# Kernel optimization log

Measured on AMD Instinct MI355X. Metric: run time of the kernel, lower is better.

## Reference

```python
import jax, jax.numpy as jnp
import numpy as np
import math
from jax import lax

B, HS, WS, C, T, TD, HH, TOPM = 8, 64, 64, 512, 77, 512, 8, 3
DH = C // HH
CONF_TH = 0.35


def _layernorm(x, w, b, eps=1e-5):
    mu = x.mean(-1, keepdims=True)
    var = ((x - mu) ** 2).mean(-1, keepdims=True)
    return (x - mu) * lax.rsqrt(var + eps) * w + b


def _l2norm(x, eps=1e-6):
    n = jnp.sqrt((x * x).sum(-1, keepdims=True))
    return x / jnp.maximum(n, eps)


def _forward(visual_features, text_features, geo_mask,
             ln1_w, ln1_b, wq, bq, wk, bk, wv, bv, wo, bo,
             gate_w, gate_b, logit_scale, alpha,
             ln2_w, ln2_b, ffn_w1, ffn_b1, ffn_w2, ffn_b2):
    Bb, Hs, Ws, Cv = visual_features.shape
    N = Hs * Ws
    # Pre-LN + flatten spatial
    x = _layernorm(visual_features, ln1_w, ln1_b).reshape(Bb, N, Cv)
    q_full = x @ wq + bq                                  # [B,N,C]
    pad_mask = jnp.abs(text_features).sum(-1) <= 1e-6     # [B,T]
    k_full = text_features @ wk + bk                      # [B,T,C]
    v_full = text_features @ wv + bv
    # per-token L2 normalize over full channel dim, then split heads
    q = _l2norm(q_full).reshape(Bb, N, HH, DH)
    k = _l2norm(k_full).reshape(Bb, T, HH, DH)
    v = v_full.reshape(Bb, T, HH, DH)
    scale = jnp.exp(jnp.clip(logit_scale, -2.0, 2.0)) / jnp.sqrt(jnp.float32(DH))
    sim = jnp.einsum('bnhd,bthd->bnht', q, k) * scale     # [B,N,H,T]
    # geo gate (4D tensor branch): log-bias on logits + multiplicative channel gate later
    gate_map = jnp.clip(geo_mask, 0.3, 1.0)               # [B,1,Hs,Ws]
    geo_gate_flat = gate_map.reshape(Bb, N, 1)            # [B,N,1]
    sim = sim + jnp.log(jnp.maximum(gate_map.reshape(Bb, N), 1e-6))[:, :, None, None]
    sim = jnp.where(pad_mask[:, None, None, :], -jnp.inf, sim)
    # Top-K sparsification before softmax (threshold at the K-th value)
    topv = lax.top_k(sim, TOPM)[0]                        # [B,N,H,K]
    sim = jnp.where(sim >= topv[..., -1:], sim, -jnp.inf)
    attn = jax.nn.softmax(sim, axis=-1)
    attn = attn / jnp.maximum(attn.sum(-1, keepdims=True), 1e-6)
    # fully-padded rows -> zero
    all_pad = pad_mask.all(axis=1)
    attn = jnp.where(all_pad[:, None, None, None], 0.0, attn)
    # confidence bypass: conf = max_prob * (1 - normalized entropy), mean over heads
    a_hn = attn.transpose(0, 2, 1, 3)                     # [B,H,N,T]
    maxp = a_hn.max(-1, keepdims=True)
    t_eff = jnp.maximum((a_hn > 0).astype(a_hn.dtype).sum(-1, keepdims=True), 2.0)
    p = jnp.maximum(a_hn, 1e-8)
    ent = jnp.maximum(-(p * jnp.log(p)).sum(-1, keepdims=True) / jnp.log(t_eff), 0.0)
    conf = jnp.clip(maxp * (1.0 - ent), 0.0, 1.0).mean(axis=1)   # [B,N,1]
    conf_scale = CONF_TH + (1.0 - CONF_TH) * jnp.clip(conf, 0.0, 1.0)
    aligned = jnp.einsum('bnht,bthd->bnhd', attn, v).reshape(Bb, N, HH * DH)
    aligned = (aligned @ wo + bo) * conf_scale
    gate = jax.nn.sigmoid(x @ gate_w + gate_b) * geo_gate_flat
    y = x + alpha * gate * aligned
    h = _layernorm(y, ln2_w, ln2_b)
    y = y + (jax.nn.gelu(h @ ffn_w1 + ffn_b1, approximate=False) @ ffn_w2 + ffn_b2)
    return y.reshape(Bb, Hs, Ws, Cv)


def setup_inputs() -> dict:
    key = jax.random.key(0)
    ks = jax.random.split(key, 16)
    def w(k, shp, fan_in):
        return (jax.random.normal(k, shp, jnp.float32) * (1.0 / math.sqrt(fan_in))).astype(jnp.float32)
    return {
        'visual_features': jax.random.normal(ks[0], (B, HS, WS, C), jnp.float32),
        'text_features':   jax.random.normal(ks[1], (B, T, TD), jnp.float32),
        'geo_mask':        jax.random.uniform(ks[2], (B, 1, HS, WS), jnp.float32),
        'ln1_w': jnp.ones((C,), jnp.float32), 'ln1_b': jnp.zeros((C,), jnp.float32),
        'wq': w(ks[3], (C, C), C),   'bq': jnp.zeros((C,), jnp.float32),
        'wk': w(ks[4], (TD, C), TD), 'bk': jnp.zeros((C,), jnp.float32),
        'wv': w(ks[5], (TD, C), TD), 'bv': jnp.zeros((C,), jnp.float32),
        'wo': w(ks[6], (C, C), C),   'bo': jnp.zeros((C,), jnp.float32),
        'gate_w': w(ks[7], (C, C), C), 'gate_b': jnp.zeros((C,), jnp.float32),
        'logit_scale': jnp.float32(math.log(1.0 / 0.07)),
        'alpha': jnp.float32(0.1),
        'ln2_w': jnp.ones((C,), jnp.float32), 'ln2_b': jnp.zeros((C,), jnp.float32),
        'ffn_w1': w(ks[8], (C, 4 * C), C),    'ffn_b1': jnp.zeros((4 * C,), jnp.float32),
        'ffn_w2': w(ks[9], (4 * C, C), 4 * C), 'ffn_b2': jnp.zeros((C,), jnp.float32),
    }


def reference(visual_features, text_features, geo_mask,
              ln1_w, ln1_b, wq, bq, wk, bk, wv, bv, wo, bo,
              gate_w, gate_b, logit_scale, alpha,
              ln2_w, ln2_b, ffn_w1, ffn_b1, ffn_w2, ffn_b2):
    return _forward(visual_features, text_features, geo_mask,
                    ln1_w, ln1_b, wq, bq, wk, bk, wv, bv, wo, bo,
                    gate_w, gate_b, logit_scale, alpha,
                    ln2_w, ln2_b, ffn_w1, ffn_b1, ffn_w2, ffn_b2)
```

## Files before the change

### kernel.cpp

```cpp
#include <hip/hip_runtime.h>
#include <hip/hip_bf16.h>
#include <math.h>

#define TT 77
#define MTOT 32768

typedef __attribute__((ext_vector_type(8))) short bf16x8;
typedef __attribute__((ext_vector_type(4))) float floatx4;

#define GPTR(p) ((const __attribute__((address_space(1))) void*)(p))
#define LPTR(p) ((__attribute__((address_space(3))) void*)(p))

__device__ __forceinline__ float wred_sum(float v) {
#pragma unroll
  for (int o = 32; o >= 1; o >>= 1) v += __shfl_xor(v, o, 64);
  return v;
}

__device__ __forceinline__ unsigned short f2bf(float f) {
  unsigned int u = __float_as_uint(f);
  unsigned int r = (u + 0x7fffu + ((u >> 16) & 1u)) >> 16;
  return (unsigned short)r;
}
__device__ __forceinline__ float bf2f(unsigned short h) {
  return __uint_as_float(((unsigned int)h) << 16);
}
__device__ __forceinline__ unsigned int cvt2bf(float a, float b) {
  unsigned int r;
  asm("v_cvt_pk_bf16_f32 %0, %1, %2" : "=v"(r) : "v"(a), "v"(b));
  return r;
}

__device__ __forceinline__ float fast_gelu(float o) {
  const float z = fabsf(o) * 0.70710678118654752f;
  const float t = __builtin_amdgcn_rcpf(fmaf(0.3275911f, z, 1.0f));
  float p = fmaf(1.061405429f, t, -1.453152027f);
  p = fmaf(p, t, 1.421413741f);
  p = fmaf(p, t, -0.284496736f);
  p = fmaf(p, t, 0.254829592f);
  p = p * t;
  const float erfz = fmaf(-p, __expf(-z * z), 1.0f);
  const float s = __builtin_copysignf(erfz, o);
  return 0.5f * o * (1.0f + s);
}

__device__ __forceinline__ float fast_sigmoid(float o) {
  return __builtin_amdgcn_rcpf(1.0f + __expf(-o));
}

__global__ __launch_bounds__(256)
void ln_bf16_kernel(const float* __restrict__ in, const float* __restrict__ gw,
                    const float* __restrict__ gb, unsigned short* __restrict__ out) {
  const int wv = threadIdx.x >> 6, lane = threadIdx.x & 63;
  const size_t row = (size_t)blockIdx.x * 4 + wv;
  const float* p = in + row * 512 + lane * 8;
  float4 a = *(const float4*)p;
  float4 b = *(const float4*)(p + 4);
  float s = a.x + a.y + a.z + a.w + b.x + b.y + b.z + b.w;
  float mu = wred_sum(s) * (1.0f / 512.0f);
  float d[8] = {a.x - mu, a.y - mu, a.z - mu, a.w - mu,
                b.x - mu, b.y - mu, b.z - mu, b.w - mu};
  float ss = 0.f;
#pragma unroll
  for (int i = 0; i < 8; ++i) ss = fmaf(d[i], d[i], ss);
  float var = wred_sum(ss) * (1.0f / 512.0f);
  float rstd = rsqrtf(var + 1e-5f);
  float4 w0 = *(const float4*)(gw + lane * 8);
  float4 w1 = *(const float4*)(gw + lane * 8 + 4);
  float4 c0 = *(const float4*)(gb + lane * 8);
  float4 c1 = *(const float4*)(gb + lane * 8 + 4);
  float o[8];
  o[0] = d[0] * rstd * w0.x + c0.x;  o[1] = d[1] * rstd * w0.y + c0.y;
  o[2] = d[2] * rstd * w0.z + c0.z;  o[3] = d[3] * rstd * w0.w + c0.w;
  o[4] = d[4] * rstd * w1.x + c1.x;  o[5] = d[5] * rstd * w1.y + c1.y;
  o[6] = d[6] * rstd * w1.z + c1.z;  o[7] = d[7] * rstd * w1.w + c1.w;
  __align__(16) unsigned short ob[8];
#pragma unroll
  for (int i = 0; i < 8; ++i) ob[i] = f2bf(o[i]);
  *(uint4*)(out + row * 512 + lane * 8) = *(const uint4*)ob;
}

__global__ __launch_bounds__(256)
void zero_ss_kernel(float* __restrict__ ssq) {
  ssq[blockIdx.x * 256 + threadIdx.x] = 0.0f;
}

__global__ __launch_bounds__(256)
void transpose_bf16_kernel(const float* __restrict__ W, unsigned short* __restrict__ WTb,
                           int K, int N) {
  __shared__ float s[32][33];
  const int tx = threadIdx.x & 31, ty = threadIdx.x >> 5;
  const int n0 = blockIdx.x * 32, k0 = blockIdx.y * 32;
#pragma unroll
  for (int j = 0; j < 4; ++j)
    s[ty + 8 * j][tx] = W[(size_t)(k0 + ty + 8 * j) * N + n0 + tx];
  __syncthreads();
#pragma unroll
  for (int j = 0; j < 4; ++j)
    WTb[(size_t)(n0 + ty + 8 * j) * K + k0 + tx] = f2bf(s[tx][ty + 8 * j]);
}

__global__ __launch_bounds__(256)
void transpose_pair_kernel(const float* __restrict__ W,
                           unsigned short* __restrict__ WTh,
                           unsigned short* __restrict__ WTl, int K, int N) {
  __shared__ float s[32][33];
  const int tx = threadIdx.x & 31, ty = threadIdx.x >> 5;
  const int n0 = blockIdx.x * 32, k0 = blockIdx.y * 32;
#pragma unroll
  for (int j = 0; j < 4; ++j)
    s[ty + 8 * j][tx] = W[(size_t)(k0 + ty + 8 * j) * N + n0 + tx];
  __syncthreads();
#pragma unroll
  for (int j = 0; j < 4; ++j) {
    const float a = s[tx][ty + 8 * j];
    const unsigned short hi = f2bf(a);
    WTh[(size_t)(n0 + ty + 8 * j) * K + k0 + tx] = hi;
    WTl[(size_t)(n0 + ty + 8 * j) * K + k0 + tx] = f2bf(a - bf2f(hi));
  }
}

__global__ __launch_bounds__(256)
void text_cvt_kernel(const float* __restrict__ text,
                     unsigned short* __restrict__ thi,
                     unsigned short* __restrict__ tlo,
                     float* __restrict__ negm) {
  const int wv = threadIdx.x >> 6, lane = threadIdx.x & 63;
  const int row = blockIdx.x * 4 + wv;
  if (row >= 616) {
    const uint4 z = {0u, 0u, 0u, 0u};
    *(uint4*)(thi + (size_t)row * 512 + lane * 8) = z;
    *(uint4*)(tlo + (size_t)row * 512 + lane * 8) = z;
    return;
  }
  const float* p = text + (size_t)row * 512 + lane * 8;
  float4 a = *(const float4*)p;
  float4 b = *(const float4*)(p + 4);
  float v[8] = {a.x, a.y, a.z, a.w, b.x, b.y, b.z, b.w};
  float ab = 0.f;
#pragma unroll
  for (int i = 0; i < 8; ++i) ab += fabsf(v[i]);
  ab = wred_sum(ab);
  __align__(16) unsigned short hb[8];
  __align__(16) unsigned short lb[8];
#pragma unroll
  for (int i = 0; i < 8; ++i) {
    hb[i] = f2bf(v[i]);
    lb[i] = f2bf(v[i] - bf2f(hb[i]));
  }
  *(uint4*)(thi + (size_t)row * 512 + lane * 8) = *(const uint4*)hb;
  *(uint4*)(tlo + (size_t)row * 512 + lane * 8) = *(const uint4*)lb;
  if (lane == 0) {
    const int bb = row / 77, t = row - bb * 77;
    negm[bb * 80 + t] = (ab <= 1e-6f) ? -INFINITY : 0.0f;
  }
}

__global__ __launch_bounds__(256)
void kv_gemm(const unsigned short* __restrict__ AH,
             const unsigned short* __restrict__ AL,
             const unsigned short* __restrict__ BH,
             const unsigned short* __restrict__ BL,
             const float* __restrict__ bk, const float* __restrict__ bv,
             float* __restrict__ outp) {
  const int K = 512;
  __shared__ __align__(16) unsigned short AsH[128 * 32];
  __shared__ __align__(16) unsigned short AsL[128 * 32];
  __shared__ __align__(16) unsigned short BsH[128 * 32];
  __shared__ __align__(16) unsigned short BsL[128 * 32];
  const int tid = threadIdx.x;
  const int wid = tid >> 6, lane = tid & 63;
  const int wr = wid >> 1, wc = wid & 1;
  const int m16 = lane & 15, quad = lane >> 4;
  const int row0 = blockIdx.y * 128, col0 = blockIdx.x * 128;

  const floatx4 zero4 = {0.f, 0.f, 0.f, 0.f};
  floatx4 acc[4][4];
#pragma unroll
  for (int i = 0; i < 4; ++i)
#pragma unroll
    for (int j = 0; j < 4; ++j) acc[i][j] = zero4;

  const int srow = tid >> 2;
  const int schunk = (tid & 3) ^ (srow & 3);
  const unsigned short* AgH = AH + (size_t)(row0 + srow) * K + schunk * 8;
  const unsigned short* AgL = AL + (size_t)(row0 + srow) * K + schunk * 8;
  const unsigned short* BgH = BH + (size_t)(col0 + srow) * K + schunk * 8;
  const unsigned short* BgL = BL + (size_t)(col0 + srow) * K + schunk * 8;
  char* AsHB = (char*)AsH + tid * 16;
  char* AsLB = (char*)AsL + tid * 16;
  char* BsHB = (char*)BsH + tid * 16;
  char* BsLB = (char*)BsL + tid * 16;
  const int rq = quad ^ (m16 & 3);
  const int aOfs = (wr * 64 + m16) * 32 + rq * 8;
  const int bOfs = (wc * 64 + m16) * 32 + rq * 8;

  for (int k0 = 0; k0 < K; k0 += 32) {
    __syncthreads();
    __builtin_amdgcn_global_load_lds(GPTR(AgH + k0), LPTR(AsHB), 16, 0, 0);
    __builtin_amdgcn_global_load_lds(GPTR(AgH + (size_t)64 * K + k0), LPTR(AsHB + 4096), 16, 0, 0);
    __builtin_amdgcn_global_load_lds(GPTR(AgL + k0), LPTR(AsLB), 16, 0, 0);
    __builtin_amdgcn_global_load_lds(GPTR(AgL + (size_t)64 * K + k0), LPTR(AsLB + 4096), 16, 0, 0);
    __builtin_amdgcn_global_load_lds(GPTR(BgH + k0), LPTR(BsHB), 16, 0, 0);
    __builtin_amdgcn_global_load_lds(GPTR(BgH + (size_t)64 * K + k0), LPTR(BsHB + 4096), 16, 0, 0);
    __builtin_amdgcn_global_load_lds(GPTR(BgL + k0), LPTR(BsLB), 16, 0, 0);
    __builtin_amdgcn_global_load_lds(GPTR(BgL + (size_t)64 * K + k0), LPTR(BsLB + 4096), 16, 0, 0);
    __syncthreads();
    bf16x8 afH[4], afL[4], bfH[4], bfL[4];
#pragma unroll
    for (int i = 0; i < 4; ++i) {
      afH[i] = *(const bf16x8*)(AsH + aOfs + i * 16 * 32);
      afL[i] = *(const bf16x8*)(AsL + aOfs + i * 16 * 32);
      bfH[i] = *(const bf16x8*)(BsH + bOfs + i * 16 * 32);
      bfL[i] = *(const bf16x8*)(BsL + bOfs + i * 16 * 32);
    }
#pragma unroll
    for (int mi = 0; mi < 4; ++mi)
#pragma unroll
      for (int ni = 0; ni < 4; ++ni) {
        acc[mi][ni] = __builtin_amdgcn_mfma_f32_16x16x32_bf16(afH[mi], bfH[ni], acc[mi][ni], 0, 0, 0);
        acc[mi][ni] = __builtin_amdgcn_mfma_f32_16x16x32_bf16(afH[mi], bfL[ni], acc[mi][ni], 0, 0, 0);
        acc[mi][ni] = __builtin_amdgcn_mfma_f32_16x16x32_bf16(afL[mi], bfH[ni], acc[mi][ni], 0, 0, 0);
      }
  }

  const float* bp = (col0 < 512) ? bk : bv;
  const int cbase = (col0 < 512) ? col0 : col0 - 512;
  float bb[4];
#pragma unroll
  for (int ni = 0; ni < 4; ++ni) bb[ni] = bp[cbase + wc * 64 + ni * 16 + m16];
#pragma unroll
  for (int mi = 0; mi < 4; ++mi)
#pragma unroll
    for (int r = 0; r < 4; ++r) {
      const int row = row0 + wr * 64 + mi * 16 + quad * 4 + r;
#pragma unroll
      for (int ni = 0; ni < 4; ++ni) {
        const int col = col0 + wc * 64 + ni * 16 + m16;
        outp[(size_t)row * 1024 + col] = acc[mi][ni][r] + bb[ni];
      }
    }
}

__global__ __launch_bounds__(256)
void knorm_kernel(const float* __restrict__ KV,
                  unsigned short* __restrict__ khb) {
  const int wv = threadIdx.x >> 6, lane = threadIdx.x & 63;
  const int row = blockIdx.x * 4 + wv;
  const float* p = KV + (size_t)row * 1024 + lane * 8;
  float4 a = *(const float4*)p;
  float4 b = *(const float4*)(p + 4);
  float v[8] = {a.x, a.y, a.z, a.w, b.x, b.y, b.z, b.w};
  float ss = 0.f;
#pragma unroll
  for (int i = 0; i < 8; ++i) ss = fmaf(v[i], v[i], ss);
  ss = wred_sum(ss);
  const float sc = 1.0f / fmaxf(sqrtf(ss), 1e-6f);
  const int bb = row / 77, t = row - bb * 77;
  const int c = lane * 8, h = c >> 6, d = c & 63;
  __align__(16) unsigned short ob[8];
#pragma unroll
  for (int i = 0; i < 8; ++i) ob[i] = f2bf(v[i] * sc);
  *(uint4*)(khb + (((size_t)bb * 8 + h) * 80 + t) * 64 + d) = *(const uint4*)ob;
}

__global__ __launch_bounds__(256)
void kpad_zero_kernel(unsigned short* __restrict__ khb, float* __restrict__ negm) {
  const int i = blockIdx.x * 256 + threadIdx.x;
  const int bh = i / 192, rem = i - bh * 192;
  const int t = 77 + rem / 64, d = rem & 63;
  khb[(((size_t)bh) * 80 + t) * 64 + d] = 0;
  if (i < 24) negm[(i / 3) * 80 + 77 + (i % 3)] = -INFINITY;
}

__global__ __launch_bounds__(256)
void sim_kernel(const unsigned short* __restrict__ qnb,
                const unsigned short* __restrict__ khb,
                const float* __restrict__ negm,
                const float* __restrict__ ssq,
                const float* __restrict__ logit_scale,
                float* __restrict__ SIM) {
  __shared__ __align__(16) unsigned short As[128 * 72];
  __shared__ __align__(16) unsigned short Bs[80 * 72];
  const int bh = blockIdx.y;
  const int b = bh >> 3, h = bh & 7;
  const int row0 = blockIdx.x * 128;
  const int tid = threadIdx.x;
  {
    const int r = tid >> 1, half = tid & 1;
    const unsigned short* src = qnb + ((size_t)b * 4096 + row0 + r) * 512 + h * 64 + half * 32;
    unsigned short* dst = As + r * 72 + half * 32;
    *(uint4*)dst = *(const uint4*)src;
    *(uint4*)(dst + 8) = *(const uint4*)(src + 8);
    *(uint4*)(dst + 16) = *(const uint4*)(src + 16);
    *(uint4*)(dst + 24) = *(const uint4*)(src + 24);
  }
  if (tid < 160) {
    const int r = tid >> 1, half = tid & 1;
    const unsigned short* src = khb + ((size_t)bh * 80 + r) * 64 + half * 32;
    unsigned short* dst = Bs + r * 72 + half * 32;
    *(uint4*)dst = *(const uint4*)src;
    *(uint4*)(dst + 8) = *(const uint4*)(src + 8);
    *(uint4*)(dst + 16) = *(const uint4*)(src + 16);
    *(uint4*)(dst + 24) = *(const uint4*)(src + 24);
  }
  __syncthreads();
  const int w = tid >> 6, lane = tid & 63;
  const int m16 = lane & 15, quad = lane >> 4;
  const unsigned short* aBase = As + (w * 32 + m16) * 72 + quad * 8;
  const unsigned short* bBase = Bs + m16 * 72 + quad * 8;
  bf16x8 af[2][2], bf[5][2];
#pragma unroll
  for (int mi = 0; mi < 2; ++mi)
#pragma unroll
    for (int kk = 0; kk < 2; ++kk)
      af[mi][kk] = *(const bf16x8*)(aBase + mi * 16 * 72 + kk * 32);
#pragma unroll
  for (int ni = 0; ni < 5; ++ni)
#pragma unroll
    for (int kk = 0; kk < 2; ++kk)
      bf[ni][kk] = *(const bf16x8*)(bBase + ni * 16 * 72 + kk * 32);
  const floatx4 zero4 = {0.f, 0.f, 0.f, 0.f};
  floatx4 acc[2][5];
#pragma unroll
  for (int mi = 0; mi < 2; ++mi)
#pragma unroll
    for (int ni = 0; ni < 5; ++ni) acc[mi][ni] = zero4;
#pragma unroll
  for (int kk = 0; kk < 2; ++kk)
#pragma unroll
    for (int mi = 0; mi < 2; ++mi)
#pragma unroll
      for (int ni = 0; ni < 5; ++ni)
        acc[mi][ni] = __builtin_amdgcn_mfma_f32_16x16x32_bf16(af[mi][kk], bf[ni][kk], acc[mi][ni], 0, 0, 0);
  const float ls = fminf(fmaxf(logit_scale[0], -2.0f), 2.0f);
  const float scale = expf(ls) * 0.125f;
  float nm[5];
#pragma unroll
  for (int ni = 0; ni < 5; ++ni) nm[ni] = negm[b * 80 + ni * 16 + m16];
  float* obase = SIM + ((size_t)bh * 4096 + row0 + w * 32 + quad * 4) * 80 + m16;
#pragma unroll
  for (int mi = 0; mi < 2; ++mi)
#pragma unroll
    for (int r = 0; r < 4; ++r) {
      const int rl = row0 + w * 32 + quad * 4 + mi * 16 + r;
      const float ssv = ssq[(size_t)b * 4096 + rl];
      const float nsc = scale / fmaxf(sqrtf(ssv), 1e-6f);
#pragma unroll
      for (int ni = 0; ni < 5; ++ni)
        obase[(size_t)(mi * 16 + r) * 80 + ni * 16] = acc[mi][ni][r] * nsc + nm[ni];
    }
}

__global__ __launch_bounds__(256)
void attn_topk_pv_kernel(const float* __restrict__ SIM,
                         const float* __restrict__ vf,
                         unsigned short* __restrict__ alignedb,
                         float* __restrict__ conf_out) {
  const int g = blockIdx.x * 256 + threadIdx.x;
  const int b = g >> 15;
  const int local = g & 32767;
  const int n = local >> 3, h = local & 7;
  const float* sp = SIM + ((size_t)(b * 8 + h) * 4096 + n) * 80;

  float m1 = -INFINITY, m2 = -INFINITY, m3 = -INFINITY, m4 = -INFINITY;
  int a1 = 0, a2 = 0, a3 = 0;
#pragma unroll
  for (int i = 0; i < 20; ++i) {
    const float4 q = ((const float4*)sp)[i];
#pragma unroll
    for (int j = 0; j < 4; ++j) {
      const float v = (j == 0) ? q.x : (j == 1) ? q.y : (j == 2) ? q.z : q.w;
      const int t = i * 4 + j;
      const bool c1 = v > m1, c2 = v > m2, c3 = v > m3, c4 = v > m4;
      m4 = c4 ? (c3 ? m3 : v) : m4;
      m3 = c3 ? (c2 ? m2 : v) : m3;
      a3 = c3 ? (c2 ? a2 : t) : a3;
      m2 = c2 ? (c1 ? m1 : v) : m2;
      a2 = c2 ? (c1 ? a1 : t) : a2;
      m1 = c1 ? v : m1;
      a1 = c1 ? t : a1;
    }
  }

  const bool dead = (m1 == -INFINITY);
  if (dead) m1 = 0.0f;
  const bool tie = (!dead) && ((m1 == m2) || (m2 == m3) || (m3 == m4));

  const float d2 = m2 - m1, d3 = m3 - m1;
  const float e2 = __expf(d2), e3 = __expf(d3);
  float s0 = 1.0f + e2 + e3;
  float s1 = ((e2 > 0.f) ? e2 * d2 : 0.f) + ((e3 > 0.f) ? e3 * d3 : 0.f);
  float cntf = 1.0f + ((e2 > 0.f) ? 1.f : 0.f) + ((e3 > 0.f) ? 1.f : 0.f);

  const float w1 = dead ? 0.f : 1.f;
  const float* v1p = vf + (size_t)(b * 77 + a1) * 1024 + h * 64;
  const float* v2p = vf + (size_t)(b * 77 + a2) * 1024 + h * 64;
  const float* v3p = vf + (size_t)(b * 77 + a3) * 1024 + h * 64;
  float4 acc[16];
#pragma unroll
  for (int i = 0; i < 16; ++i) {
    const float4 x1 = ((const float4*)v1p)[i];
    const float4 x2 = ((const float4*)v2p)[i];
    const float4 x3 = ((const float4*)v3p)[i];
    float4 r;
    r.x = fmaf(e3, x3.x, fmaf(e2, x2.x, w1 * x1.x));
    r.y = fmaf(e3, x3.y, fmaf(e2, x2.y, w1 * x1.y));
    r.z = fmaf(e3, x3.z, fmaf(e2, x2.z, w1 * x1.z));
    r.w = fmaf(e3, x3.w, fmaf(e2, x2.w, w1 * x1.w));
    acc[i] = r;
  }

  if (__any(tie)) {
    if (tie) {
      s0 = 0.f; s1 = 0.f; cntf = 0.f;
#pragma unroll
      for (int i = 0; i < 16; ++i) acc[i] = (float4){0.f, 0.f, 0.f, 0.f};
      for (int t = 0; t < 80; ++t) {
        const float v = sp[t];
        if (v >= m3) {
          const float e = expf(v - m1);
          if (e > 0.f) {
            s0 += e; s1 = fmaf(e, v - m1, s1); cntf += 1.f;
            const float4* vp = (const float4*)(vf + (size_t)(b * 77 + t) * 1024 + h * 64);
#pragma unroll
            for (int i = 0; i < 16; ++i) {
              const float4 x = vp[i];
              acc[i].x = fmaf(e, x.x, acc[i].x);
              acc[i].y = fmaf(e, x.y, acc[i].y);
              acc[i].z = fmaf(e, x.z, acc[i].z);
              acc[i].w = fmaf(e, x.w, acc[i].w);
            }
          }
        }
      }
    }
  }

  const float inv = 1.0f / s0;
  const float entn = (__logf(s0) - s1 * inv) + (77.0f - cntf) * 1.8420681e-7f;
  const float ent = fmaxf(entn / __logf(fmaxf(cntf, 2.0f)), 0.0f);
  float conf_h = fminf(fmaxf(inv * (1.0f - ent), 0.0f), 1.0f);
  if (dead) conf_h = 0.f;
  float cs = conf_h;
  cs += __shfl_xor(cs, 1, 64);
  cs += __shfl_xor(cs, 2, 64);
  cs += __shfl_xor(cs, 4, 64);
  if (h == 0) {
    const float cm = fminf(fmaxf(cs * 0.125f, 0.0f), 1.0f);
    conf_out[(size_t)b * 4096 + n] = 0.35f + 0.65f * cm;
  }

  unsigned short* op = alignedb + ((size_t)b * 4096 + n) * 512 + h * 64;
#pragma unroll
  for (int i = 0; i < 8; ++i) {
    const float4 lo = acc[2 * i], hi = acc[2 * i + 1];
    uint4 pk;
    pk.x = cvt2bf(lo.x * inv, lo.y * inv);
    pk.y = cvt2bf(lo.z * inv, lo.w * inv);
    pk.z = cvt2bf(hi.x * inv, hi.y * inv);
    pk.w = cvt2bf(hi.z * inv, hi.w * inv);
    *(uint4*)(op + i * 8) = pk;
  }
}

template <int EPI, int KC>
__global__ __launch_bounds__(256)
void mfma_gemm(const unsigned short* __restrict__ A,
               const unsigned short* __restrict__ WT,
               const float* __restrict__ bias,
               void* __restrict__ outv, int M, int N,
               const unsigned short* __restrict__ e0b,
               const float* __restrict__ e1f,
               const float* __restrict__ e2f,
               const float* __restrict__ scf) {
  __shared__ __align__(16) unsigned short As[128 * 32];
  __shared__ __align__(16) unsigned short Bs[128 * 32];
  const int tid = threadIdx.x;
  const int wid = tid >> 6, lane = tid & 63;
  const int wr = wid >> 1, wc = wid & 1;
  const int m16 = lane & 15, quad = lane >> 4;

  const int nwg = gridDim.x * gridDim.y;
  const int orig = blockIdx.y * gridDim.x + blockIdx.x;
  const int qq = nwg >> 3, rr = nwg & 7;
  const int xcd = orig & 7, base = orig >> 3;
  const int logical = (xcd < rr ? xcd * (qq + 1) : rr * (qq + 1) + (xcd - rr) * qq) + base;
  const int bx = logical % gridDim.x, by = logical / gridDim.x;
  const int row0 = by * 128, col0 = bx * 128;

  const floatx4 zero4 = {0.f, 0.f, 0.f, 0.f};
  floatx4 acc[4][4];
#pragma unroll
  for (int i = 0; i < 4; ++i)
#pragma unroll
    for (int j = 0; j < 4; ++j) acc[i][j] = zero4;

  const int srow = tid >> 2;
  const int schunk = (tid & 3) ^ (srow & 3);
  const unsigned short* Ag = A + (size_t)(row0 + srow) * KC + schunk * 8;
  const unsigned short* Bg = WT + (size_t)(col0 + srow) * KC + schunk * 8;
  char* AsB = (char*)As + tid * 16;
  char* BsB = (char*)Bs + tid * 16;
  const int rq = quad ^ (m16 & 3);
  const unsigned short* aP = As + (wr * 64 + m16) * 32 + rq * 8;
  const unsigned short* bP = Bs + (wc * 64 + m16) * 32 + rq * 8;

  for (int k0 = 0; k0 < KC; k0 += 32) {
    __syncthreads();
    __builtin_amdgcn_global_load_lds(GPTR(Ag + k0), LPTR(AsB), 16, 0, 0);
    __builtin_amdgcn_global_load_lds(GPTR(Ag + (size_t)64 * KC + k0), LPTR(AsB + 4096), 16, 0, 0);
    __builtin_amdgcn_global_load_lds(GPTR(Bg + k0), LPTR(BsB), 16, 0, 0);
    __builtin_amdgcn_global_load_lds(GPTR(Bg + (size_t)64 * KC + k0), LPTR(BsB + 4096), 16, 0, 0);
    __syncthreads();
    bf16x8 af[4], bfr[4];
#pragma unroll
    for (int i = 0; i < 4; ++i) {
      af[i] = *(const bf16x8*)(aP + i * 16 * 32);
      bfr[i] = *(const bf16x8*)(bP + i * 16 * 32);
    }
#pragma unroll
    for (int mi = 0; mi < 4; ++mi)
#pragma unroll
      for (int ni = 0; ni < 4; ++ni)
        acc[mi][ni] = __builtin_amdgcn_mfma_f32_16x16x32_bf16(af[mi], bfr[ni], acc[mi][ni], 0, 0, 0);
  }

  float* outf = (float*)outv;
  unsigned short* outb = (unsigned short*)outv;
  const unsigned short* albf = (const unsigned short*)e1f;
  float bb[4];
#pragma unroll
  for (int ni = 0; ni < 4; ++ni) bb[ni] = bias[col0 + wc * 64 + ni * 16 + m16];
  const float alphav = (EPI == 2) ? scf[0] : 0.f;

#pragma unroll
  for (int mi = 0; mi < 4; ++mi) {
#pragma unroll
    for (int r = 0; r < 4; ++r) {
      const int row = row0 + wr * 64 + mi * 16 + quad * 4 + r;
      float o[4];
#pragma unroll
      for (int ni = 0; ni < 4; ++ni) o[ni] = acc[mi][ni][r] + bb[ni];
      const size_t basei = (size_t)row * N + col0 + wc * 64 + m16;

      if (EPI == 5) {
        const unsigned int p01 = cvt2bf(o[0], o[1]);
        const unsigned int p23 = cvt2bf(o[2], o[3]);
        outb[basei] = (unsigned short)p01;
        outb[basei + 16] = (unsigned short)(p01 >> 16);
        outb[basei + 32] = (unsigned short)p23;
        outb[basei + 48] = (unsigned short)(p23 >> 16);
        float p = fmaf(o[0], o[0], fmaf(o[1], o[1], fmaf(o[2], o[2], o[3] * o[3])));
        p += __shfl_xor(p, 1, 64);
        p += __shfl_xor(p, 2, 64);
        p += __shfl_xor(p, 4, 64);
        p += __shfl_xor(p, 8, 64);
        if (m16 == 0) atomicAdd(const_cast<float*>(e1f) + row, p);
      } else if (EPI == 3) {
        const unsigned int p01 = cvt2bf(fast_gelu(o[0]), fast_gelu(o[1]));
        const unsigned int p23 = cvt2bf(fast_gelu(o[2]), fast_gelu(o[3]));
        outb[basei] = (unsigned short)p01;
        outb[basei + 16] = (unsigned short)(p01 >> 16);
        outb[basei + 32] = (unsigned short)p23;
        outb[basei + 48] = (unsigned short)(p23 >> 16);
      } else if (EPI == 1) {
        const float rowscale = e1f[row];
        const unsigned int p01 = cvt2bf(o[0] * rowscale, o[1] * rowscale);
        const unsigned int p23 = cvt2bf(o[2] * rowscale, o[3] * rowscale);
        outb[basei] = (unsigned short)p01;
        outb[basei + 16] = (unsigned short)(p01 >> 16);
        outb[basei + 32] = (unsigned short)p23;
        outb[basei + 48] = (unsigned short)(p23 >> 16);
      } else if (EPI == 2) {
        const float geo = fminf(fmaxf(e2f[row], 0.3f), 1.0f);
#pragma unroll
        for (int ni = 0; ni < 4; ++ni) {
          const size_t idx = basei + ni * 16;
          const float x = bf2f(e0b[idx]);
          const float al = bf2f(albf[idx]);
          const float sg = fast_sigmoid(o[ni]);
          outf[idx] = x + alphav * sg * geo * al;
        }
      } else {
#pragma unroll
        for (int ni = 0; ni < 4; ++ni) {
          const size_t idx = basei + ni * 16;
          outf[idx] = o[ni] + e1f[idx];
        }
      }
    }
  }
}

extern "C" void kernel_launch(void* const* d_in, const int* in_sizes, int n_in,
                              void* d_out, int out_size, void* d_ws, size_t ws_size,
                              hipStream_t stream) {
  const float* visual = (const float*)d_in[0];
  const float* text   = (const float*)d_in[1];
  const float* geo    = (const float*)d_in[2];
  const float* ln1_w  = (const float*)d_in[3];
  const float* ln1_b  = (const float*)d_in[4];
  const float* wq     = (const float*)d_in[5];
  const float* bq     = (const float*)d_in[6];
  const float* wk     = (const float*)d_in[7];
  const float* bk     = (const float*)d_in[8];
  const float* wvw    = (const float*)d_in[9];
  const float* bv     = (const float*)d_in[10];
  const float* wo     = (const float*)d_in[11];
  const float* bo     = (const float*)d_in[12];
  const float* gate_w = (const float*)d_in[13];
  const float* gate_b = (const float*)d_in[14];
  const float* logit_scale = (const float*)d_in[15];
  const float* alpha  = (const float*)d_in[16];
  const float* ln2_w  = (const float*)d_in[17];
  const float* ln2_b  = (const float*)d_in[18];
  const float* ffn_w1 = (const float*)d_in[19];
  const float* ffn_b1 = (const float*)d_in[20];
  const float* ffn_w2 = (const float*)d_in[21];
  const float* ffn_b2 = (const float*)d_in[22];
  float* out = (float*)d_out;

  char* ws = (char*)d_ws;
  float* R0            = (float*)ws;
  float* BUF2          = (float*)(ws + 88080384);
  unsigned short* Xb   = (unsigned short*)(ws + 155189248);
  unsigned short* QNb  = (unsigned short*)(ws + 188743680);
  unsigned short* wqT  = (unsigned short*)(ws + 222298112);
  unsigned short* woT  = wqT + 262144;
  unsigned short* gateT = woT + 262144;
  unsigned short* w1T  = gateT + 262144;
  unsigned short* w2T  = w1T + 1048576;
  unsigned short* KHb  = w2T + 1048576;
  float* NEGM = (float*)(ws + 230146048);
  float* CONF = (float*)(ws + 230148608);
  float* SSQ  = (float*)(ws + 230279680);

  float* KV            = (float*)(ws + 88080384);
  unsigned short* THi  = (unsigned short*)(ws + 88080384 + 2621440);
  unsigned short* TLo  = THi + 640 * 512;
  unsigned short* WKVh = TLo + 640 * 512;
  unsigned short* WKVl = WKVh + 1024 * 512;

  float* SIM = R0;
  unsigned short* ALb = QNb;

  transpose_bf16_kernel<<<dim3(16, 16), 256, 0, stream>>>(wq, wqT, 512, 512);
  transpose_bf16_kernel<<<dim3(16, 16), 256, 0, stream>>>(wo, woT, 512, 512);
  transpose_bf16_kernel<<<dim3(16, 16), 256, 0, stream>>>(gate_w, gateT, 512, 512);
  transpose_bf16_kernel<<<dim3(64, 16), 256, 0, stream>>>(ffn_w1, w1T, 512, 2048);
  transpose_bf16_kernel<<<dim3(16, 64), 256, 0, stream>>>(ffn_w2, w2T, 2048, 512);
  transpose_pair_kernel<<<dim3(16, 16), 256, 0, stream>>>(wk, WKVh, WKVl, 512, 512);
  transpose_pair_kernel<<<dim3(16, 16), 256, 0, stream>>>(wvw, WKVh + 512 * 512, WKVl + 512 * 512, 512, 512);

  ln_bf16_kernel<<<MTOT / 4, 256, 0, stream>>>(visual, ln1_w, ln1_b, Xb);
  zero_ss_kernel<<<128, 256, 0, stream>>>(SSQ);
  text_cvt_kernel<<<160, 256, 0, stream>>>(text, THi, TLo, NEGM);
  kv_gemm<<<dim3(8, 5), 256, 0, stream>>>(THi, TLo, WKVh, WKVl, bk, bv, KV);
  knorm_kernel<<<154, 256, 0, stream>>>(KV, KHb);
  kpad_zero_kernel<<<48, 256, 0, stream>>>(KHb, NEGM);
  mfma_gemm<5, 512><<<dim3(4, 256), 256, 0, stream>>>(Xb, wqT, bq, QNb, MTOT, 512,
                                                      nullptr, SSQ, nullptr, nullptr);
  sim_kernel<<<dim3(32, 64), 256, 0, stream>>>(QNb, KHb, NEGM, SSQ, logit_scale, SIM);
  attn_topk_pv_kernel<<<1024, 256, 0, stream>>>(SIM, KV + 512, ALb, CONF);
  unsigned short* AOb = (unsigned short*)R0;
  mfma_gemm<1, 512><<<dim3(4, 256), 256, 0, stream>>>(ALb, woT, bo, AOb, MTOT, 512,
                                                      nullptr, CONF, nullptr, nullptr);
  mfma_gemm<2, 512><<<dim3(4, 256), 256, 0, stream>>>(Xb, gateT, gate_b, BUF2, MTOT, 512,
                                                      Xb, (const float*)AOb, geo, alpha);
  ln_bf16_kernel<<<MTOT / 4, 256, 0, stream>>>(BUF2, ln2_w, ln2_b, Xb);
  unsigned short* GCH = (unsigned short*)R0;
  for (int ch = 0; ch < 2; ++ch) {
    const size_t off = (size_t)ch * 16384;
    mfma_gemm<3, 512><<<dim3(16, 128), 256, 0, stream>>>(Xb + off * 512, w1T, ffn_b1, GCH,
                                                         16384, 2048,
                                                         nullptr, nullptr, nullptr, nullptr);
    mfma_gemm<4, 2048><<<dim3(4, 128), 256, 0, stream>>>(GCH, w2T, ffn_b2, out + off * 512,
                                                         16384, 512,
                                                         nullptr, BUF2 + off * 512, nullptr, nullptr);
  }
}
```

Measured before the change: 606.2 us.

## Interleave SIM layout across heads and stream top-3 value gather

```diff
diff --git a/kernel.cpp b/kernel.cpp
--- a/kernel.cpp
+++ b/kernel.cpp
@@ -338,7 +338,8 @@
   float nm[5];
 #pragma unroll
   for (int ni = 0; ni < 5; ++ni) nm[ni] = negm[b * 80 + ni * 16 + m16];
-  float* obase = SIM + ((size_t)bh * 4096 + row0 + w * 32 + quad * 4) * 80 + m16;
+  float* obase = SIM + ((size_t)b * 4096 + row0 + w * 32 + quad * 4) * 640 + h * 4 + (m16 & 3);
+  const int jb = m16 >> 2;
 #pragma unroll
   for (int mi = 0; mi < 2; ++mi)
 #pragma unroll
@@ -348,7 +349,7 @@
       const float nsc = scale / fmaxf(sqrtf(ssv), 1e-6f);
 #pragma unroll
       for (int ni = 0; ni < 5; ++ni)
-        obase[(size_t)(mi * 16 + r) * 80 + ni * 16] = acc[mi][ni][r] * nsc + nm[ni];
+        obase[(size_t)(mi * 16 + r) * 640 + (ni * 4 + jb) * 32] = acc[mi][ni][r] * nsc + nm[ni];
     }
 }
 
@@ -361,13 +362,13 @@
   const int b = g >> 15;
   const int local = g & 32767;
   const int n = local >> 3, h = local & 7;
-  const float* sp = SIM + ((size_t)(b * 8 + h) * 4096 + n) * 80;
+  const float* sp = SIM + ((size_t)b * 4096 + n) * 640 + h * 4;
 
   float m1 = -INFINITY, m2 = -INFINITY, m3 = -INFINITY, m4 = -INFINITY;
   int a1 = 0, a2 = 0, a3 = 0;
 #pragma unroll
   for (int i = 0; i < 20; ++i) {
-    const float4 q = ((const float4*)sp)[i];
+    const float4 q = *(const float4*)(sp + i * 32);
 #pragma unroll
     for (int j = 0; j < 4; ++j) {
       const float v = (j == 0) ? q.x : (j == 1) ? q.y : (j == 2) ? q.z : q.w;
@@ -393,31 +394,16 @@
   float s1 = ((e2 > 0.f) ? e2 * d2 : 0.f) + ((e3 > 0.f) ? e3 * d3 : 0.f);
   float cntf = 1.0f + ((e2 > 0.f) ? 1.f : 0.f) + ((e3 > 0.f) ? 1.f : 0.f);
 
-  const float w1 = dead ? 0.f : 1.f;
-  const float* v1p = vf + (size_t)(b * 77 + a1) * 1024 + h * 64;
-  const float* v2p = vf + (size_t)(b * 77 + a2) * 1024 + h * 64;
-  const float* v3p = vf + (size_t)(b * 77 + a3) * 1024 + h * 64;
-  float4 acc[16];
-#pragma unroll
-  for (int i = 0; i < 16; ++i) {
-    const float4 x1 = ((const float4*)v1p)[i];
-    const float4 x2 = ((const float4*)v2p)[i];
-    const float4 x3 = ((const float4*)v3p)[i];
-    float4 r;
-    r.x = fmaf(e3, x3.x, fmaf(e2, x2.x, w1 * x1.x));
-    r.y = fmaf(e3, x3.y, fmaf(e2, x2.y, w1 * x1.y));
-    r.z = fmaf(e3, x3.z, fmaf(e2, x2.z, w1 * x1.z));
-    r.w = fmaf(e3, x3.w, fmaf(e2, x2.w, w1 * x1.w));
-    acc[i] = r;
-  }
+  unsigned short* op = alignedb + ((size_t)b * 4096 + n) * 512 + h * 64;
 
   if (__any(tie)) {
     if (tie) {
       s0 = 0.f; s1 = 0.f; cntf = 0.f;
+      float4 acc[16];
 #pragma unroll
       for (int i = 0; i < 16; ++i) acc[i] = (float4){0.f, 0.f, 0.f, 0.f};
       for (int t = 0; t < 80; ++t) {
-        const float v = sp[t];
+        const float v = sp[(t >> 2) * 32 + (t & 3)];
         if (v >= m3) {
           const float e = expf(v - m1);
           if (e > 0.f) {
@@ -433,6 +419,17 @@
             }
           }
         }
+      }
+      const float invt = 1.0f / s0;
+#pragma unroll
+      for (int i = 0; i < 8; ++i) {
+        const float4 lo = acc[2 * i], hi = acc[2 * i + 1];
+        uint4 pk;
+        pk.x = cvt2bf(lo.x * invt, lo.y * invt);
+        pk.y = cvt2bf(lo.z * invt, lo.w * invt);
+        pk.z = cvt2bf(hi.x * invt, hi.y * invt);
+        pk.w = cvt2bf(hi.z * invt, hi.w * invt);
+        *(uint4*)(op + i * 8) = pk;
       }
     }
   }
@@ -451,16 +448,36 @@
     conf_out[(size_t)b * 4096 + n] = 0.35f + 0.65f * cm;
   }
 
-  unsigned short* op = alignedb + ((size_t)b * 4096 + n) * 512 + h * 64;
-#pragma unroll
-  for (int i = 0; i < 8; ++i) {
-    const float4 lo = acc[2 * i], hi = acc[2 * i + 1];
-    uint4 pk;
-    pk.x = cvt2bf(lo.x * inv, lo.y * inv);
-    pk.y = cvt2bf(lo.z * inv, lo.w * inv);
-    pk.z = cvt2bf(hi.x * inv, hi.y * inv);
-    pk.w = cvt2bf(hi.z * inv, hi.w * inv);
-    *(uint4*)(op + i * 8) = pk;
+  if (!tie) {
+    const float wA = dead ? 0.f : inv;
+    const float wB = e2 * inv, wC = e3 * inv;
+    const float* v1p = vf + (size_t)(b * 77 + a1) * 1024 + h * 64;
+    const float* v2p = vf + (size_t)(b * 77 + a2) * 1024 + h * 64;
+    const float* v3p = vf + (size_t)(b * 77 + a3) * 1024 + h * 64;
+#pragma unroll
+    for (int i = 0; i < 8; ++i) {
+      const float4 a0 = ((const float4*)v1p)[2 * i];
+      const float4 a1v = ((const float4*)v1p)[2 * i + 1];
+      const float4 b0 = ((const float4*)v2p)[2 * i];
+      const float4 b1 = ((const float4*)v2p)[2 * i + 1];
+      const float4 c0 = ((const float4*)v3p)[2 * i];
+      const float4 c1 = ((const float4*)v3p)[2 * i + 1];
+      float4 r0, r1;
+      r0.x = fmaf(wC, c0.x, fmaf(wB, b0.x, wA * a0.x));
+      r0.y = fmaf(wC, c0.y, fmaf(wB, b0.y, wA * a0.y));
+      r0.z = fmaf(wC, c0.z, fmaf(wB, b0.z, wA * a0.z));
+      r0.w = fmaf(wC, c0.w, fmaf(wB, b0.w, wA * a0.w));
+      r1.x = fmaf(wC, c1.x, fmaf(wB, b1.x, wA * a1v.x));
+      r1.y = fmaf(wC, c1.y, fmaf(wB, b1.y, wA * a1v.y));
+      r1.z = fmaf(wC, c1.z, fmaf(wB, b1.z, wA * a1v.z));
+      r1.w = fmaf(wC, c1.w, fmaf(wB, b1.w, wA * a1v.w));
+      uint4 pk;
+      pk.x = cvt2bf(r0.x, r0.y);
+      pk.y = cvt2bf(r0.z, r0.w);
+      pk.z = cvt2bf(r1.x, r1.y);
+      pk.w = cvt2bf(r1.z, r1.w);
+      *(uint4*)(op + i * 8) = pk;
+    }
   }
 }
 
```

Result: no change. 616.9 us (+1.8%).
